# Kernel optimization log

Hardware: AMD Instinct MI355X
Metric: run time of the kernel (lower is better)

The kernel has to match this reference:

```python
import jax, jax.numpy as jnp
import numpy as np

NUM_ITERS = 3
NUM_HEADS = 4
EPS = 1e-8
LN_EPS = 1e-5


def _layernorm(x, w, b):
    mu = jnp.mean(x, axis=-1, keepdims=True)
    var = jnp.mean(jnp.square(x - mu), axis=-1, keepdims=True)
    return (x - mu) * jax.lax.rsqrt(var + LN_EPS) * w + b


def setup_inputs() -> dict:
    key = jax.random.key(0)
    ks = jax.random.split(key, 12)
    B, K, D, Q, Hm = 64, 4096, 256, 8, 512
    s = 0.02
    return {
        "inputs": jax.random.normal(ks[0], (B, K, D), jnp.float32),
        "slots_init": jax.random.normal(ks[1], (B, Q, D), jnp.float32),
        "Wq": jax.random.normal(ks[2], (D, D), jnp.float32) * s,
        "Wk": jax.random.normal(ks[3], (D, D), jnp.float32) * s,
        "Wv": jax.random.normal(ks[4], (D, D), jnp.float32) * s,
        "ln_in_w": jnp.ones((D,), jnp.float32),
        "ln_in_b": jnp.zeros((D,), jnp.float32),
        "ln_slots_w": jnp.ones((D,), jnp.float32),
        "ln_slots_b": jnp.zeros((D,), jnp.float32),
        "ln_mlp_w": jnp.ones((D,), jnp.float32),
        "ln_mlp_b": jnp.zeros((D,), jnp.float32),
        "gru_Wih": jax.random.normal(ks[5], (3 * D, D), jnp.float32) * s,
        "gru_Whh": jax.random.normal(ks[6], (3 * D, D), jnp.float32) * s,
        "gru_bih": jnp.zeros((3 * D,), jnp.float32),
        "gru_bhh": jnp.zeros((3 * D,), jnp.float32),
        "mlp_W1": jax.random.normal(ks[7], (D, Hm), jnp.float32) * s,
        "mlp_b1": jnp.zeros((Hm,), jnp.float32),
        "mlp_W2": jax.random.normal(ks[8], (Hm, D), jnp.float32) * s,
        "mlp_b2": jnp.zeros((D,), jnp.float32),
    }


def reference(inputs, slots_init, Wq, Wk, Wv, ln_in_w, ln_in_b, ln_slots_w,
              ln_slots_b, ln_mlp_w, ln_mlp_b, gru_Wih, gru_Whh, gru_bih,
              gru_bhh, mlp_W1, mlp_b1, mlp_W2, mlp_b2):
    B, K, D = inputs.shape
    Q = slots_init.shape[1]
    H = NUM_HEADS
    dh = D // H
    scale = dh ** -0.5

    x = _layernorm(inputs, ln_in_w, ln_in_b)
    k = (x @ Wk).reshape(B, K, H, dh).transpose(0, 2, 1, 3) * scale  # [B,H,K,dh]
    v = (x @ Wv).reshape(B, K, H, dh).transpose(0, 2, 1, 3)          # [B,H,K,dh]

    slots = slots_init
    attn = None
    for _ in range(NUM_ITERS):
        slots_prev = slots
        s_n = _layernorm(slots, ln_slots_w, ln_slots_b)
        q = (s_n @ Wq).reshape(B, Q, H, dh).transpose(0, 2, 1, 3)    # [B,H,Q,dh]
        logits = jnp.einsum('bhkd,bhqd->bhkq', k, q)                 # [B,H,K,Q]
        # softmax jointly over (heads, slots) per kv position
        attn = jax.nn.softmax(
            logits.transpose(0, 2, 1, 3).reshape(B, K, H * Q), axis=-1
        ).reshape(B, K, H, Q).transpose(0, 2, 1, 3)                  # [B,H,K,Q]
        attn = attn + EPS
        attn = attn / jnp.sum(attn, axis=2, keepdims=True)           # renorm over K
        updates = jnp.einsum('bhkq,bhkd->bqhd', attn, v).reshape(B, Q, D)

        # GRU cell (PyTorch gate order: r, z, n)
        u = updates.reshape(-1, D)
        h = slots_prev.reshape(-1, D)
        gi = u @ gru_Wih.T + gru_bih
        gh = h @ gru_Whh.T + gru_bhh
        i_r, i_z, i_n = jnp.split(gi, 3, axis=-1)
        h_r, h_z, h_n = jnp.split(gh, 3, axis=-1)
        r = jax.nn.sigmoid(i_r + h_r)
        z = jax.nn.sigmoid(i_z + h_z)
        n = jnp.tanh(i_n + r * h_n)
        slots = ((1.0 - z) * n + z * h).reshape(B, Q, D)

        m = _layernorm(slots, ln_mlp_w, ln_mlp_b)
        slots = slots + jax.nn.relu(m @ mlp_W1 + mlp_b1) @ mlp_W2 + mlp_b2

    return slots, attn.mean(axis=1).transpose(0, 2, 1)  # [B,Q,D], [B,Q,K]
```

## Files before the change

### kernel.cpp

```cpp
#include <hip/hip_runtime.h>

#define B   64
#define KK  4096
#define D   256
#define Q   8
#define H   4
#define DH  64
#define HQ  32
#define HM  512
#define NCH 16
#define CHK 256
#define EPS 1e-8f
#define LNE 1e-5f
#define SCALE 0.125f

typedef short bf16x8 __attribute__((ext_vector_type(8)));
typedef float f32x4 __attribute__((ext_vector_type(4)));

#define MFMA __builtin_amdgcn_mfma_f32_16x16x32_bf16

__device__ __forceinline__ float bf2f(unsigned short u) {
    unsigned int x = ((unsigned int)u) << 16;
    float f; __builtin_memcpy(&f, &x, 4); return f;
}
__device__ __forceinline__ unsigned short f2bf(float f) {
    unsigned int x; __builtin_memcpy(&x, &f, 4);
    unsigned int lsb = (x >> 16) & 1u;
    x += 0x7fffu + lsb;
    return (unsigned short)(x >> 16);
}

__device__ __forceinline__ void gload16(const void* g, void* l) {
    __builtin_amdgcn_global_load_lds(
        (const __attribute__((address_space(1))) unsigned int*)g,
        (__attribute__((address_space(3))) unsigned int*)l, 16, 0, 0);
}

__global__ __launch_bounds__(256) void k_prep(
    const float* __restrict__ Wk, const float* __restrict__ Wv,
    const float* __restrict__ gWih, const float* __restrict__ gWhh,
    const float* __restrict__ W1, const float* __restrict__ W2,
    const float* __restrict__ Wq, const float* __restrict__ s0,
    unsigned short* __restrict__ WkvT, unsigned short* __restrict__ Wihbf,
    unsigned short* __restrict__ Whhbf, unsigned short* __restrict__ W1T,
    unsigned short* __restrict__ W2T, unsigned short* __restrict__ WqT,
    float* __restrict__ slots)
{
    const int blk = blockIdx.x, t = threadIdx.x;
    if (blk < 512) {
        const int c = blk;
        const float v = (c < 256) ? Wk[(size_t)t * 256 + c] * SCALE
                                  : Wv[(size_t)t * 256 + (c - 256)];
        WkvT[(size_t)c * 256 + t] = f2bf(v);
    } else if (blk < 1280) {
        const int i = (blk - 512) * 256 + t;
        Wihbf[i] = f2bf(gWih[i]);
    } else if (blk < 2048) {
        const int i = (blk - 1280) * 256 + t;
        Whhbf[i] = f2bf(gWhh[i]);
    } else if (blk < 2560) {
        const int nn = blk - 2048;
        W1T[(size_t)nn * 256 + t] = f2bf(W1[(size_t)t * 512 + nn]);
    } else if (blk < 2816) {
        const int nn = blk - 2560;
        W2T[(size_t)nn * 512 + t]       = f2bf(W2[(size_t)t * 256 + nn]);
        W2T[(size_t)nn * 512 + 256 + t] = f2bf(W2[(size_t)(256 + t) * 256 + nn]);
    } else if (blk < 3072) {
        const int nn = blk - 2816;
        WqT[(size_t)nn * 256 + t] = f2bf(Wq[(size_t)t * 256 + nn]);
    } else {
        const int i = (blk - 3072) * 256 + t;
        slots[i] = s0[i];
    }
}

__global__ __launch_bounds__(256) void k1_mfma(
    const float* __restrict__ inp, const unsigned short* __restrict__ WkvT,
    const float* __restrict__ lnw, const float* __restrict__ lnb,
    unsigned short* __restrict__ kpk, unsigned short* __restrict__ vpk)
{
    __shared__ char smem[49152];
    char* abase = smem;
    char* bb0 = smem + 32768;
    char* bb1 = smem;
    const int t = threadIdx.x, w = t >> 6, l = t & 63;
    const size_t row0 = (size_t)blockIdx.x * 64;
    const int b_blk = blockIdx.x >> 6;
    const int kbase = (blockIdx.x & 63) * 64;

    auto stageB = [&](int n2, char* dst) {
#pragma unroll
        for (int i = 0; i < 4; ++i) {
            const int seg = w * 4 + i;
            const int r = seg * 2 + (l >> 5);
            const int off = ((l & 31) * 16) ^ ((r & 7) << 4);
            gload16((const char*)WkvT + ((size_t)n2 * 32 + r) * 512 + off, dst + seg * 1024);
        }
    };
    stageB(0, bb0);

    float4 xv[16];
#pragma unroll
    for (int i = 0; i < 16; ++i)
        xv[i] = ((const float4*)(inp + (row0 + w * 16 + i) * D))[l];
    const float4 w4 = ((const float4*)lnw)[l];
    const float4 b4 = ((const float4*)lnb)[l];
#pragma unroll
    for (int i = 0; i < 16; ++i) {
        const int r = w * 16 + i;
        float4 x = xv[i];
        float s  = x.x + x.y + x.z + x.w;
        float ss = x.x*x.x + x.y*x.y + x.z*x.z + x.w*x.w;
#pragma unroll
        for (int off = 32; off; off >>= 1) { s += __shfl_xor(s, off); ss += __shfl_xor(ss, off); }
        const float mu = s * (1.f / 256.f);
        const float rs = rsqrtf(ss * (1.f / 256.f) - mu * mu + LNE);
        ushort4 pk;
        pk.x = f2bf((x.x - mu) * rs * w4.x + b4.x);
        pk.y = f2bf((x.y - mu) * rs * w4.y + b4.y);
        pk.z = f2bf((x.z - mu) * rs * w4.z + b4.z);
        pk.w = f2bf((x.w - mu) * rs * w4.w + b4.w);
        *(ushort4*)(abase + r * 512 + ((l * 8) ^ ((r & 7) << 4))) = pk;
    }
    __syncthreads();

    const int arow = w * 16 + (l & 15);
    const char* ap = abase + arow * 512;
    const int asw = (l & 7) << 4;
    bf16x8 af[8];
#pragma unroll
    for (int kk = 0; kk < 8; ++kk)
        af[kk] = *(const bf16x8*)(ap + ((kk * 64 + (l >> 4) * 16) ^ asw));
    __syncthreads();
    stageB(1, bb1);

    const int lg = l >> 4;
    const f32x4 fz = {0.f, 0.f, 0.f, 0.f};
    for (int n2 = 0; n2 < 16; ++n2) {
        const char* bbase = (n2 & 1) ? bb1 : bb0;
        f32x4 acc[2] = {fz, fz};
        if (n2 < 8) {
#pragma unroll
            for (int kk = 0; kk < 8; ++kk) {
                const int koff = kk * 64 + lg * 16;
#pragma unroll
                for (int nf = 0; nf < 2; ++nf) {
                    const int brow = nf * 16 + (l & 15);
                    const bf16x8 bf_ = *(const bf16x8*)(bbase + brow * 512 + (koff ^ ((brow & 7) << 4)));
                    acc[nf] = MFMA(bf_, af[kk], acc[nf], 0, 0, 0);
                }
            }
            const int kt16 = (kbase >> 4) + w;
#pragma unroll
            for (int nf = 0; nf < 2; ++nf) {
                unsigned short* kp = kpk
                    + ((((size_t)b_blk * 256 + kt16) * 8 + n2) * 512)
                    + ((l & 15) + ((nf * 2 + (lg >> 1)) << 4)) * 8 + (lg & 1) * 4;
                ushort4 pk;
                pk.x = f2bf(acc[nf][0]); pk.y = f2bf(acc[nf][1]);
                pk.z = f2bf(acc[nf][2]); pk.w = f2bf(acc[nf][3]);
                *(ushort4*)kp = pk;
            }
        } else {
#pragma unroll
            for (int kk = 0; kk < 8; ++kk) {
                const int koff = kk * 64 + lg * 16;
#pragma unroll
                for (int nf = 0; nf < 2; ++nf) {
                    const int brow = nf * 16 + (l & 15);
                    const bf16x8 bf_ = *(const bf16x8*)(bbase + brow * 512 + (koff ^ ((brow & 7) << 4)));
                    acc[nf] = MFMA(af[kk], bf_, acc[nf], 0, 0, 0);
                }
            }
            const int kt32 = (kbase >> 5) + (w >> 1);
#pragma unroll
            for (int nf = 0; nf < 2; ++nf) {
                const int dt16 = (n2 - 8) * 2 + nf;
                unsigned short* vp = vpk
                    + ((((size_t)b_blk * 128 + kt32) * 16 + dt16) * 512)
                    + ((l & 15) + (((w & 1) * 2 + (lg >> 1)) << 4)) * 8 + (lg & 1) * 4;
                ushort4 pk;
                pk.x = f2bf(acc[nf][0]); pk.y = f2bf(acc[nf][1]);
                pk.z = f2bf(acc[nf][2]); pk.w = f2bf(acc[nf][3]);
                *(ushort4*)vp = pk;
            }
        }
        __syncthreads();
        if (n2 < 14) stageB(n2 + 2, (n2 & 1) ? bb1 : bb0);
    }
}

__global__ __launch_bounds__(256) void k2_qproj(
    const float* __restrict__ slots, const float* __restrict__ Wq,
    const float* __restrict__ lnw, const float* __restrict__ lnb, float* __restrict__ qbuf)
{
    const int row = blockIdx.x, t = threadIdx.x;
    __shared__ float sn[256];
    __shared__ float red[8];
    const float x = slots[(size_t)row * D + t];
    float mu, rs;
    {
        float s = x, ss = x * x;
#pragma unroll
        for (int off = 32; off; off >>= 1) { s += __shfl_xor(s, off); ss += __shfl_xor(ss, off); }
        if ((t & 63) == 0) { red[t >> 6] = s; red[4 + (t >> 6)] = ss; }
        __syncthreads();
        const float S  = red[0] + red[1] + red[2] + red[3];
        const float SS = red[4] + red[5] + red[6] + red[7];
        mu = S * (1.f / 256.f);
        rs = rsqrtf(SS * (1.f / 256.f) - mu * mu + LNE);
    }
    sn[t] = (x - mu) * rs * lnw[t] + lnb[t];
    __syncthreads();
    float acc = 0.f;
    for (int d = 0; d < 256; ++d) acc = fmaf(sn[d], Wq[(size_t)d * 256 + t], acc);
    qbuf[(size_t)row * D + t] = acc;
}

__global__ __launch_bounds__(256) void k_attn(
    const unsigned short* __restrict__ kpk, const unsigned short* __restrict__ vpk,
    const float* __restrict__ qbuf, float* __restrict__ updp,
    float* __restrict__ denp, float* __restrict__ pbuf, int write_p)
{
    __shared__ unsigned short psm[2][2048];
    __shared__ float dred[4][32];
    const int t = threadIdx.x, w = t >> 6, l = t & 63;
    const int b = blockIdx.x >> 4, chunk = blockIdx.x & 15;
    const int k0g = chunk * CHK;
    const int n = l & 15, lg = l >> 4;

    bf16x8 qf[2][2];
#pragma unroll
    for (int p = 0; p < 2; ++p) {
        const int h = p * 2 + (n >> 3);
        const float* qb = qbuf + ((size_t)b * Q + (n & 7)) * D;
#pragma unroll
        for (int j = 0; j < 2; ++j) {
            const int dbase = (h * 2 + j) * 32 + lg * 8;
            short tmp[8];
#pragma unroll
            for (int e = 0; e < 8; ++e) tmp[e] = (short)f2bf(qb[dbase + e]);
            __builtin_memcpy(&qf[p][j], tmp, 16);
        }
    }
    const bf16x8 ZV = {0,0,0,0,0,0,0,0};
    const f32x4 fz = {0.f,0.f,0.f,0.f};
    f32x4 pv[2][4];
#pragma unroll
    for (int mt = 0; mt < 2; ++mt)
#pragma unroll
        for (int nf = 0; nf < 4; ++nf) pv[mt][nf] = fz;
    float den0 = 0.f, den1 = 0.f;

    const unsigned short* kb0 = kpk + (((size_t)(b * 256 + chunk * 16 + w)) * 8) * 512 + l * 8;
    const unsigned short* vb0 = vpk + (((size_t)(b * 128 + chunk * 8) * 16) + w * 4) * 512 + l * 8;

    for (int tile = 0; tile < 4; ++tile) {
        bf16x8 kf[8];
#pragma unroll
        for (int kk = 0; kk < 8; ++kk)
            kf[kk] = *(const bf16x8*)(kb0 + (size_t)tile * 16384 + kk * 512);
        f32x4 lac[2] = {fz, fz};
#pragma unroll
        for (int kk = 0; kk < 8; ++kk) {
            const int p = kk >> 2;
            const bool on = (((kk & 3) >> 1) == (n >> 3));
            const bf16x8 bq = on ? qf[p][kk & 1] : ZV;
            if (p == 0) lac[0] = MFMA(kf[kk], bq, lac[0], 0, 0, 0);
            else        lac[1] = MFMA(kf[kk], bq, lac[1], 0, 0, 0);
        }
#pragma unroll
        for (int reg = 0; reg < 4; ++reg) {
            float m = fmaxf(lac[0][reg], lac[1][reg]);
#pragma unroll
            for (int off = 8; off; off >>= 1) m = fmaxf(m, __shfl_xor(m, off));
            const float e0 = __expf(lac[0][reg] - m);
            const float e1 = __expf(lac[1][reg] - m);
            float se = e0 + e1;
#pragma unroll
            for (int off = 8; off; off >>= 1) se += __shfl_xor(se, off);
            const float inv = 1.f / se;
            lac[0][reg] = e0 * inv; lac[1][reg] = e1 * inv;
            den0 += lac[0][reg];    den1 += lac[1][reg];
        }
        char* pb = (char*)psm[tile & 1];
        const int kb = w * 16 + lg * 4;
        {
            ushort4 p0, p1;
            p0.x = f2bf(lac[0][0]); p0.y = f2bf(lac[0][1]); p0.z = f2bf(lac[0][2]); p0.w = f2bf(lac[0][3]);
            p1.x = f2bf(lac[1][0]); p1.y = f2bf(lac[1][1]); p1.z = f2bf(lac[1][2]); p1.w = f2bf(lac[1][3]);
            *(ushort4*)(pb + n * 128 + ((kb * 2) ^ ((n & 7) << 4))) = p0;
            *(ushort4*)(pb + (16 + n) * 128 + ((kb * 2) ^ ((n & 7) << 4))) = p1;
        }
        if (write_p) {
            float* pp = pbuf + ((size_t)b * KK + k0g + tile * 64 + kb) * HQ;
#pragma unroll
            for (int reg = 0; reg < 4; ++reg) {
                pp[(size_t)reg * HQ + n] = lac[0][reg];
                pp[(size_t)reg * HQ + 16 + n] = lac[1][reg];
            }
        }
        __syncthreads();
#pragma unroll
        for (int kkp = 0; kkp < 2; ++kkp) {
            const int koff = kkp * 64 + lg * 16;
            const bf16x8 a0 = *(const bf16x8*)(pb + n * 128 + (koff ^ ((n & 7) << 4)));
            const bf16x8 a1 = *(const bf16x8*)(pb + (16 + n) * 128 + (koff ^ ((n & 7) << 4)));
#pragma unroll
            for (int nf = 0; nf < 4; ++nf) {
                const bf16x8 bv = *(const bf16x8*)(vb0 + (tile * 32 + kkp * 16 + nf) * 512);
                pv[0][nf] = MFMA(a0, bv, pv[0][nf], 0, 0, 0);
                pv[1][nf] = MFMA(a1, bv, pv[1][nf], 0, 0, 0);
            }
        }
    }

    den0 += __shfl_xor(den0, 16); den0 += __shfl_xor(den0, 32);
    den1 += __shfl_xor(den1, 16); den1 += __shfl_xor(den1, 32);
    if (l < 16) { dred[w][l] = den0; dred[w][16 + l] = den1; }
    __syncthreads();
    if (t < 32)
        denp[((size_t)b * NCH + chunk) * HQ + t] =
            dred[0][t] + dred[1][t] + dred[2][t] + dred[3][t];

    if ((lg >> 1) == (w & 1)) {
        const int mt = w >> 1;
#pragma unroll
        for (int nf = 0; nf < 4; ++nf) {
#pragma unroll
            for (int reg = 0; reg < 4; ++reg) {
                const int q = (lg & 1) * 4 + reg;
                updp[(((size_t)b * NCH + chunk) * Q + q) * D + w * 64 + nf * 16 + n] = pv[mt][nf][reg];
            }
        }
    }
}

__device__ __forceinline__ void ln_rows(const f32x4 sv[4], char* dstA, float* red,
    const float* __restrict__ lnw, const float* __restrict__ lnb,
    int w, int n, int lg, int col0)
{
    float ps[4], pq[4];
#pragma unroll
    for (int r = 0; r < 4; ++r) {
        float s = 0.f, q2 = 0.f;
#pragma unroll
        for (int nf = 0; nf < 4; ++nf) { const float v = sv[nf][r]; s += v; q2 += v * v; }
#pragma unroll
        for (int off = 1; off < 16; off <<= 1) { s += __shfl_xor(s, off); q2 += __shfl_xor(q2, off); }
        ps[r] = s; pq[r] = q2;
    }
    if (n == 0) {
#pragma unroll
        for (int r = 0; r < 4; ++r) {
            red[(lg * 4 + r) * 8 + w * 2]     = ps[r];
            red[(lg * 4 + r) * 8 + w * 2 + 1] = pq[r];
        }
    }
    __syncthreads();
    float mu[4], rs[4];
#pragma unroll
    for (int r = 0; r < 4; ++r) {
        const int rowm = lg * 4 + r;
        const float S  = red[rowm*8+0] + red[rowm*8+2] + red[rowm*8+4] + red[rowm*8+6];
        const float SS = red[rowm*8+1] + red[rowm*8+3] + red[rowm*8+5] + red[rowm*8+7];
        mu[r] = S * (1.f / 256.f);
        rs[r] = rsqrtf(SS * (1.f / 256.f) - mu[r] * mu[r] + LNE);
    }
#pragma unroll
    for (int nf = 0; nf < 4; ++nf) {
        const int col = col0 + nf * 16;
        const float wv = lnw[col], bv = lnb[col];
#pragma unroll
        for (int r = 0; r < 4; ++r) {
            const int rowm = lg * 4 + r;
            const float mval = (sv[nf][r] - mu[r]) * rs[r] * wv + bv;
            *(unsigned short*)(dstA + rowm * 512 + ((col * 2) ^ ((rowm & 7) << 4))) = f2bf(mval);
        }
    }
}

__global__ __launch_bounds__(256) void k_slot(
    const float* __restrict__ updp, const float* __restrict__ denp,
    float* __restrict__ slots,
    const unsigned short* __restrict__ Wihbf, const unsigned short* __restrict__ Whhbf,
    const float* __restrict__ bih, const float* __restrict__ bhh,
    const unsigned short* __restrict__ W1T, const float* __restrict__ b1,
    const unsigned short* __restrict__ W2T, const float* __restrict__ b2,
    const float* __restrict__ lnmw, const float* __restrict__ lnmb,
    const unsigned short* __restrict__ WqT,
    const float* __restrict__ lnsw, const float* __restrict__ lnsb,
    float* __restrict__ qbuf)
{
    __shared__ char sm[34304];
    unsigned short* uA = (unsigned short*)(sm);
    unsigned short* hA = (unsigned short*)(sm + 8192);
    float* hf32        = (float*)(sm + 16384);
    char*  hidA        = sm + 16384;
    float* dsum        = (float*)(sm + 33280);
    float* red         = (float*)(sm + 33536);
    const int t = threadIdx.x, w = t >> 6, l = t & 63;
    const int n = l & 15, lg = l >> 4;
    const int R0 = blockIdx.x * 16;
    const f32x4 fz = {0.f, 0.f, 0.f, 0.f};

    {
        float us[16];
#pragma unroll
        for (int m = 0; m < 16; ++m) {
            const int gr = R0 + m, bb = gr >> 3, q = gr & 7;
            float s = 0.f;
#pragma unroll
            for (int c = 0; c < 16; ++c)
                s += updp[(((size_t)(bb * 16 + c)) * 8 + q) * 256 + t];
            us[m] = s;
        }
        if (t < 64) {
            const int m = t >> 2, h = t & 3;
            const int gr = R0 + m, bb = gr >> 3, q = gr & 7;
            float s = 0.f;
#pragma unroll
            for (int c = 0; c < 16; ++c)
                s += denp[(size_t)(bb * 16 + c) * 32 + h * 8 + q];
            dsum[m * 4 + h] = s;
        }
#pragma unroll
        for (int m = 0; m < 16; ++m) {
            const float hv = slots[(size_t)(R0 + m) * 256 + t];
            hf32[m * 264 + t] = hv;
            *(unsigned short*)((char*)hA + m * 512 + ((t * 2) ^ ((m & 7) << 4))) = f2bf(hv);
        }
        __syncthreads();
        const int h = t >> 6;
#pragma unroll
        for (int m = 0; m < 16; ++m) {
            const float inv = 1.f / (dsum[m * 4 + h] + (float)KK * EPS);
            *(unsigned short*)((char*)uA + m * 512 + ((t * 2) ^ ((m & 7) << 4))) = f2bf(us[m] * inv);
        }
    }
    __syncthreads();

    f32x4 sv[4];
    {
        f32x4 ai0[4], ai1[4], ai2[4];
#pragma unroll
        for (int nf = 0; nf < 4; ++nf) { ai0[nf] = fz; ai1[nf] = fz; ai2[nf] = fz; }
#pragma unroll
        for (int kk = 0; kk < 8; ++kk) {
            const bf16x8 au = *(const bf16x8*)((char*)uA + n * 512 + ((kk * 64 + lg * 16) ^ ((n & 7) << 4)));
            const int kidx = kk * 32 + lg * 8;
#pragma unroll
            for (int nf = 0; nf < 4; ++nf) {
                const int col = w * 64 + nf * 16 + n;
                const bf16x8 br = *(const bf16x8*)(Wihbf + (size_t)col * 256 + kidx);
                const bf16x8 bz = *(const bf16x8*)(Wihbf + (size_t)(256 + col) * 256 + kidx);
                const bf16x8 bn = *(const bf16x8*)(Wihbf + (size_t)(512 + col) * 256 + kidx);
                ai0[nf] = MFMA(au, br, ai0[nf], 0, 0, 0);
                ai1[nf] = MFMA(au, bz, ai1[nf], 0, 0, 0);
                ai2[nf] = MFMA(au, bn, ai2[nf], 0, 0, 0);
            }
        }
        f32x4 ah0[4], ah1[4], ah2[4];
#pragma unroll
        for (int nf = 0; nf < 4; ++nf) { ah0[nf] = fz; ah1[nf] = fz; ah2[nf] = fz; }
#pragma unroll
        for (int kk = 0; kk < 8; ++kk) {
            const bf16x8 ah_ = *(const bf16x8*)((char*)hA + n * 512 + ((kk * 64 + lg * 16) ^ ((n & 7) << 4)));
            const int kidx = kk * 32 + lg * 8;
#pragma unroll
            for (int nf = 0; nf < 4; ++nf) {
                const int col = w * 64 + nf * 16 + n;
                const bf16x8 cr = *(const bf16x8*)(Whhbf + (size_t)col * 256 + kidx);
                const bf16x8 cz = *(const bf16x8*)(Whhbf + (size_t)(256 + col) * 256 + kidx);
                const bf16x8 cn = *(const bf16x8*)(Whhbf + (size_t)(512 + col) * 256 + kidx);
                ah0[nf] = MFMA(ah_, cr, ah0[nf], 0, 0, 0);
                ah1[nf] = MFMA(ah_, cz, ah1[nf], 0, 0, 0);
                ah2[nf] = MFMA(ah_, cn, ah2[nf], 0, 0, 0);
            }
        }
#pragma unroll
        for (int nf = 0; nf < 4; ++nf) {
            const int col = w * 64 + nf * 16 + n;
            const float br_ = bih[col], bz_ = bih[256 + col], bn_ = bih[512 + col];
            const float cr_ = bhh[col], cz_ = bhh[256 + col], cn_ = bhh[512 + col];
#pragma unroll
            for (int r = 0; r < 4; ++r) {
                const int rowm = lg * 4 + r;
                const float ir = ai0[nf][r] + br_, iz = ai1[nf][r] + bz_, inn = ai2[nf][r] + bn_;
                const float hr = ah0[nf][r] + cr_, hz = ah1[nf][r] + cz_, hn = ah2[nf][r] + cn_;
                const float rg = 1.f / (1.f + __expf(-(ir + hr)));
                const float zg = 1.f / (1.f + __expf(-(iz + hz)));
                const float ng = tanhf(inn + rg * hn);
                const float h0v = hf32[rowm * 264 + col];
                sv[nf][r] = (1.f - zg) * ng + zg * h0v;
            }
        }
    }
    ln_rows(sv, (char*)uA, red, lnmw, lnmb, w, n, lg, w * 64 + n);
    __syncthreads();

    {
        f32x4 m1[8];
#pragma unroll
        for (int nf = 0; nf < 8; ++nf) m1[nf] = fz;
#pragma unroll
        for (int kk = 0; kk < 8; ++kk) {
            const bf16x8 a = *(const bf16x8*)((char*)uA + n * 512 + ((kk * 64 + lg * 16) ^ ((n & 7) << 4)));
            const int kidx = kk * 32 + lg * 8;
#pragma unroll
            for (int nf = 0; nf < 8; ++nf) {
                const int colh = w * 128 + nf * 16 + n;
                const bf16x8 bb = *(const bf16x8*)(W1T + (size_t)colh * 256 + kidx);
                m1[nf] = MFMA(a, bb, m1[nf], 0, 0, 0);
            }
        }
        __syncthreads();
#pragma unroll
        for (int nf = 0; nf < 8; ++nf) {
            const int colh = w * 128 + nf * 16 + n;
            const float bb = b1[colh];
#pragma unroll
            for (int r = 0; r < 4; ++r) {
                const int rowm = lg * 4 + r;
                *(unsigned short*)(hidA + rowm * 1024 + ((colh * 2) ^ ((rowm & 7) << 4)))
                    = f2bf(fmaxf(m1[nf][r] + bb, 0.f));
            }
        }
    }
    __syncthreads();

    {
        f32x4 m2[4];
#pragma unroll
        for (int nf = 0; nf < 4; ++nf) m2[nf] = fz;
#pragma unroll
        for (int kk = 0; kk < 16; ++kk) {
            const bf16x8 a = *(const bf16x8*)(hidA + n * 1024 + ((kk * 64 + lg * 16) ^ ((n & 7) << 4)));
            const int kidx = kk * 32 + lg * 8;
#pragma unroll
            for (int nf = 0; nf < 4; ++nf) {
                const int col = w * 64 + nf * 16 + n;
                const bf16x8 bb = *(const bf16x8*)(W2T + (size_t)col * 512 + kidx);
                m2[nf] = MFMA(a, bb, m2[nf], 0, 0, 0);
            }
        }
#pragma unroll
        for (int nf = 0; nf < 4; ++nf) {
            const int col = w * 64 + nf * 16 + n;
            const float bb = b2[col];
#pragma unroll
            for (int r = 0; r < 4; ++r) {
                const int rowm = lg * 4 + r;
                const float v = m2[nf][r] + bb + sv[nf][r];
                sv[nf][r] = v;
                slots[(size_t)(R0 + rowm) * 256 + col] = v;
            }
        }
    }
    ln_rows(sv, (char*)hA, red, lnsw, lnsb, w, n, lg, w * 64 + n);
    __syncthreads();

    {
        f32x4 qa[4];
#pragma unroll
        for (int nf = 0; nf < 4; ++nf) qa[nf] = fz;
#pragma unroll
        for (int kk = 0; kk < 8; ++kk) {
            const bf16x8 a = *(const bf16x8*)((char*)hA + n * 512 + ((kk * 64 + lg * 16) ^ ((n & 7) << 4)));
            const int kidx = kk * 32 + lg * 8;
#pragma unroll
            for (int nf = 0; nf < 4; ++nf) {
                const int col = w * 64 + nf * 16 + n;
                const bf16x8 bb = *(const bf16x8*)(WqT + (size_t)col * 256 + kidx);
                qa[nf] = MFMA(a, bb, qa[nf], 0, 0, 0);
            }
        }
#pragma unroll
        for (int nf = 0; nf < 4; ++nf) {
            const int col = w * 64 + nf * 16 + n;
#pragma unroll
            for (int r = 0; r < 4; ++r)
                qbuf[(size_t)(R0 + lg * 4 + r) * 256 + col] = qa[nf][r];
        }
    }
}

__global__ void k_den(const float* __restrict__ denp, float* __restrict__ invden)
{
    const int b = blockIdx.x, t = threadIdx.x;
    float s = 0.f;
#pragma unroll
    for (int c = 0; c < NCH; ++c) s += denp[((size_t)b * NCH + c) * HQ + t];
    invden[b * HQ + t] = 1.f / (s + (float)KK * EPS);
}

__global__ void k7_copy(const float* __restrict__ s, float* __restrict__ o)
{
    const int i = blockIdx.x * 256 + threadIdx.x;
    o[i] = s[i];
}

__global__ __launch_bounds__(256) void k7_attnout(
    const float* __restrict__ pbuf, const float* __restrict__ invden, float* __restrict__ out2)
{
    const int blk = blockIdx.x;
    const int b = blk >> 4;
    const int kk0 = (blk & 15) * 256;
    __shared__ float ps[256][33];
    __shared__ float inv[32];
    const int t = threadIdx.x;
    const float* pp = pbuf + ((size_t)b * KK + kk0) * HQ;
    for (int i = 0; i < 32; ++i) {
        const int idx = i * 256 + t;
        ps[idx >> 5][idx & 31] = pp[idx];
    }
    if (t < 32) inv[t] = invden[b * HQ + t];
    __syncthreads();
    float* o = out2 + (size_t)b * Q * KK + kk0 + t;
#pragma unroll
    for (int q = 0; q < 8; ++q) {
        float v = 0.f;
#pragma unroll
        for (int hh = 0; hh < 4; ++hh)
            v += (ps[t][hh * 8 + q] + EPS) * inv[hh * 8 + q];
        o[(size_t)q * KK] = v * 0.25f;
    }
}

extern "C" void kernel_launch(void* const* d_in, const int* in_sizes, int n_in,
                              void* d_out, int out_size, void* d_ws, size_t ws_size,
                              hipStream_t stream)
{
    const float* inputs  = (const float*)d_in[0];
    const float* slots0  = (const float*)d_in[1];
    const float* Wq      = (const float*)d_in[2];
    const float* Wk      = (const float*)d_in[3];
    const float* Wv      = (const float*)d_in[4];
    const float* ln_in_w = (const float*)d_in[5];
    const float* ln_in_b = (const float*)d_in[6];
    const float* ln_s_w  = (const float*)d_in[7];
    const float* ln_s_b  = (const float*)d_in[8];
    const float* ln_m_w  = (const float*)d_in[9];
    const float* ln_m_b  = (const float*)d_in[10];
    const float* gWih    = (const float*)d_in[11];
    const float* gWhh    = (const float*)d_in[12];
    const float* gbih    = (const float*)d_in[13];
    const float* gbhh    = (const float*)d_in[14];
    const float* W1      = (const float*)d_in[15];
    const float* b1      = (const float*)d_in[16];
    const float* W2      = (const float*)d_in[17];
    const float* b2      = (const float*)d_in[18];

    char* p = (char*)d_ws;
    unsigned short* kpk   = (unsigned short*)p; p += (size_t)B * KK * D * 2;
    unsigned short* vpk   = (unsigned short*)p; p += (size_t)B * KK * D * 2;
    float* pbuf   = (float*)p; p += (size_t)B * KK * HQ * 4;
    float* updp   = (float*)p; p += (size_t)B * NCH * Q * D * 4;
    float* denp   = (float*)p; p += (size_t)B * NCH * HQ * 4;
    float* invden = (float*)p; p += (size_t)B * HQ * 4;
    float* qbuf   = (float*)p; p += (size_t)B * Q * D * 4;
    float* slots  = (float*)p; p += (size_t)B * Q * D * 4;
    unsigned short* WkvT  = (unsigned short*)p; p += (size_t)512 * 256 * 2;
    unsigned short* Wihbf = (unsigned short*)p; p += (size_t)768 * 256 * 2;
    unsigned short* Whhbf = (unsigned short*)p; p += (size_t)768 * 256 * 2;
    unsigned short* W1T   = (unsigned short*)p; p += (size_t)HM * 256 * 2;
    unsigned short* W2T   = (unsigned short*)p; p += (size_t)256 * HM * 2;
    unsigned short* WqT   = (unsigned short*)p; p += (size_t)256 * 256 * 2;

    k_prep<<<3584, 256, 0, stream>>>(Wk, Wv, gWih, gWhh, W1, W2, Wq, slots0,
                                     WkvT, Wihbf, Whhbf, W1T, W2T, WqT, slots);
    k1_mfma<<<(B * KK) / 64, 256, 0, stream>>>(inputs, WkvT, ln_in_w, ln_in_b, kpk, vpk);
    k2_qproj<<<B * Q, 256, 0, stream>>>(slots, Wq, ln_s_w, ln_s_b, qbuf);
    for (int it = 0; it < 3; ++it) {
        k_attn<<<B * NCH, 256, 0, stream>>>(kpk, vpk, qbuf, updp, denp, pbuf, (it == 2) ? 1 : 0);
        k_slot<<<32, 256, 0, stream>>>(updp, denp, slots, Wihbf, Whhbf, gbih, gbhh,
                                       W1T, b1, W2T, b2, ln_m_w, ln_m_b, WqT,
                                       ln_s_w, ln_s_b, qbuf);
    }
    k_den<<<B, 32, 0, stream>>>(denp, invden);
    k7_copy<<<(B * Q * D) / 256, 256, 0, stream>>>(slots, (float*)d_out);
    k7_attnout<<<B * (KK / 256), 256, 0, stream>>>(pbuf, invden, (float*)d_out + (size_t)B * Q * D);
}
```

Measured before the change: 551.6 us.

## Fold input layernorm into K/V projection epilogue, prefetch V, drop small kernels

The input layernorm's affine weights and mean subtraction are folded algebraically into pre-packed projection weights. Column sums and bias vectors are applied in the MFMA epilogue, so k1 feeds raw bf16 inputs and loads B tiles from a pre-swizzled layout with less LDS. k_attn prefetches V fragments into registers alongside K and drops the softmax max-subtraction, which risks overflow if logits are large. The k_den and copy kernels are removed by fusing the denominator reduction into k7_attnout and writing the final slots directly from k_slot.

```diff
diff --git a/kernel.cpp b/kernel.cpp
--- a/kernel.cpp
+++ b/kernel.cpp
@@ -38,91 +38,96 @@
 
 __global__ __launch_bounds__(256) void k_prep(
     const float* __restrict__ Wk, const float* __restrict__ Wv,
+    const float* __restrict__ lnw, const float* __restrict__ lnb,
     const float* __restrict__ gWih, const float* __restrict__ gWhh,
     const float* __restrict__ W1, const float* __restrict__ W2,
     const float* __restrict__ Wq, const float* __restrict__ s0,
-    unsigned short* __restrict__ WkvT, unsigned short* __restrict__ Wihbf,
-    unsigned short* __restrict__ Whhbf, unsigned short* __restrict__ W1T,
-    unsigned short* __restrict__ W2T, unsigned short* __restrict__ WqT,
-    float* __restrict__ slots)
+    unsigned short* __restrict__ wpk, float* __restrict__ cs, float* __restrict__ b2v,
+    unsigned short* __restrict__ Wihbf, unsigned short* __restrict__ Whhbf,
+    unsigned short* __restrict__ W1T, unsigned short* __restrict__ W2T,
+    unsigned short* __restrict__ WqT, float* __restrict__ slots)
 {
     const int blk = blockIdx.x, t = threadIdx.x;
-    if (blk < 512) {
-        const int c = blk;
-        const float v = (c < 256) ? Wk[(size_t)t * 256 + c] * SCALE
-                                  : Wv[(size_t)t * 256 + (c - 256)];
-        WkvT[(size_t)c * 256 + t] = f2bf(v);
-    } else if (blk < 1280) {
-        const int i = (blk - 512) * 256 + t;
+    if (blk < 256) {
+        const int ct = blk >> 3, kt = blk & 7;
+#pragma unroll
+        for (int e2 = 0; e2 < 2; ++e2) {
+            const int i = t * 2 + e2;
+            const int lane = i >> 3, e = i & 7;
+            const int col = ct * 16 + (lane & 15);
+            const int k = kt * 32 + (lane >> 4) * 8 + e;
+            const float wv = lnw[k];
+            const float v = (col < 256) ? wv * Wk[(size_t)k * 256 + col] * SCALE
+                                        : wv * Wv[(size_t)k * 256 + (col - 256)];
+            wpk[(size_t)blk * 512 + i] = f2bf(v);
+        }
+    } else if (blk < 258) {
+        const int c = (blk - 256) * 256 + t;
+        float s1 = 0.f, s2 = 0.f;
+        for (int k = 0; k < 256; ++k) {
+            const float wraw = (c < 256) ? Wk[(size_t)k * 256 + c] * SCALE
+                                         : Wv[(size_t)k * 256 + (c - 256)];
+            s1 += lnw[k] * wraw;
+            s2 += lnb[k] * wraw;
+        }
+        cs[c] = s1; b2v[c] = s2;
+    } else if (blk < 1026) {
+        const int i = (blk - 258) * 256 + t;
         Wihbf[i] = f2bf(gWih[i]);
-    } else if (blk < 2048) {
-        const int i = (blk - 1280) * 256 + t;
+    } else if (blk < 1794) {
+        const int i = (blk - 1026) * 256 + t;
         Whhbf[i] = f2bf(gWhh[i]);
-    } else if (blk < 2560) {
-        const int nn = blk - 2048;
+    } else if (blk < 2306) {
+        const int nn = blk - 1794;
         W1T[(size_t)nn * 256 + t] = f2bf(W1[(size_t)t * 512 + nn]);
-    } else if (blk < 2816) {
-        const int nn = blk - 2560;
+    } else if (blk < 2562) {
+        const int nn = blk - 2306;
         W2T[(size_t)nn * 512 + t]       = f2bf(W2[(size_t)t * 256 + nn]);
         W2T[(size_t)nn * 512 + 256 + t] = f2bf(W2[(size_t)(256 + t) * 256 + nn]);
-    } else if (blk < 3072) {
-        const int nn = blk - 2816;
+    } else if (blk < 2818) {
+        const int nn = blk - 2562;
         WqT[(size_t)nn * 256 + t] = f2bf(Wq[(size_t)t * 256 + nn]);
     } else {
-        const int i = (blk - 3072) * 256 + t;
+        const int i = (blk - 2818) * 256 + t;
         slots[i] = s0[i];
     }
 }
 
 __global__ __launch_bounds__(256) void k1_mfma(
-    const float* __restrict__ inp, const unsigned short* __restrict__ WkvT,
-    const float* __restrict__ lnw, const float* __restrict__ lnb,
+    const float* __restrict__ inp, const unsigned short* __restrict__ wpk,
+    const float* __restrict__ cs, const float* __restrict__ b2v,
     unsigned short* __restrict__ kpk, unsigned short* __restrict__ vpk)
 {
-    __shared__ char smem[49152];
+    __shared__ char smem[32768];
     char* abase = smem;
-    char* bb0 = smem + 32768;
-    char* bb1 = smem;
+    char* bb0 = smem;
+    char* bb1 = smem + 16384;
     const int t = threadIdx.x, w = t >> 6, l = t & 63;
     const size_t row0 = (size_t)blockIdx.x * 64;
     const int b_blk = blockIdx.x >> 6;
     const int kbase = (blockIdx.x & 63) * 64;
-
-    auto stageB = [&](int n2, char* dst) {
-#pragma unroll
-        for (int i = 0; i < 4; ++i) {
-            const int seg = w * 4 + i;
-            const int r = seg * 2 + (l >> 5);
-            const int off = ((l & 31) * 16) ^ ((r & 7) << 4);
-            gload16((const char*)WkvT + ((size_t)n2 * 32 + r) * 512 + off, dst + seg * 1024);
-        }
-    };
-    stageB(0, bb0);
+    const int lg = l >> 4;
 
     float4 xv[16];
 #pragma unroll
     for (int i = 0; i < 16; ++i)
         xv[i] = ((const float4*)(inp + (row0 + w * 16 + i) * D))[l];
-    const float4 w4 = ((const float4*)lnw)[l];
-    const float4 b4 = ((const float4*)lnb)[l];
+    float rsA = 0.f, muA = 0.f;
 #pragma unroll
     for (int i = 0; i < 16; ++i) {
         const int r = w * 16 + i;
-        float4 x = xv[i];
+        const float4 x = xv[i];
         float s  = x.x + x.y + x.z + x.w;
         float ss = x.x*x.x + x.y*x.y + x.z*x.z + x.w*x.w;
 #pragma unroll
         for (int off = 32; off; off >>= 1) { s += __shfl_xor(s, off); ss += __shfl_xor(ss, off); }
         const float mu = s * (1.f / 256.f);
         const float rs = rsqrtf(ss * (1.f / 256.f) - mu * mu + LNE);
+        if ((l & 15) == i) { rsA = rs; muA = rs * mu; }
         ushort4 pk;
-        pk.x = f2bf((x.x - mu) * rs * w4.x + b4.x);
-        pk.y = f2bf((x.y - mu) * rs * w4.y + b4.y);
-        pk.z = f2bf((x.z - mu) * rs * w4.z + b4.z);
-        pk.w = f2bf((x.w - mu) * rs * w4.w + b4.w);
+        pk.x = f2bf(x.x); pk.y = f2bf(x.y); pk.z = f2bf(x.z); pk.w = f2bf(x.w);
         *(ushort4*)(abase + r * 512 + ((l * 8) ^ ((r & 7) << 4))) = pk;
     }
-    __syncthreads();
 
     const int arow = w * 16 + (l & 15);
     const char* ap = abase + arow * 512;
@@ -130,11 +135,26 @@
     bf16x8 af[8];
 #pragma unroll
     for (int kk = 0; kk < 8; ++kk)
-        af[kk] = *(const bf16x8*)(ap + ((kk * 64 + (l >> 4) * 16) ^ asw));
-    __syncthreads();
-    stageB(1, bb1);
-
-    const int lg = l >> 4;
+        af[kk] = *(const bf16x8*)(ap + ((kk * 64 + lg * 16) ^ asw));
+    float rsV[4], muV[4];
+#pragma unroll
+    for (int r = 0; r < 4; ++r) {
+        rsV[r] = __shfl(rsA, lg * 4 + r);
+        muV[r] = __shfl(muA, lg * 4 + r);
+    }
+    __syncthreads();
+
+    auto stageB = [&](int n2, char* dst) {
+#pragma unroll
+        for (int i = 0; i < 4; ++i) {
+            const int seg = w * 4 + i;
+            gload16((const char*)wpk + (size_t)n2 * 16384 + seg * 1024 + l * 16,
+                    dst + seg * 1024);
+        }
+    };
+    stageB(0, bb0); stageB(1, bb1);
+    __syncthreads();
+
     const f32x4 fz = {0.f, 0.f, 0.f, 0.f};
     for (int n2 = 0; n2 < 16; ++n2) {
         const char* bbase = (n2 & 1) ? bb1 : bb0;
@@ -142,46 +162,51 @@
         if (n2 < 8) {
 #pragma unroll
             for (int kk = 0; kk < 8; ++kk) {
-                const int koff = kk * 64 + lg * 16;
 #pragma unroll
                 for (int nf = 0; nf < 2; ++nf) {
-                    const int brow = nf * 16 + (l & 15);
-                    const bf16x8 bf_ = *(const bf16x8*)(bbase + brow * 512 + (koff ^ ((brow & 7) << 4)));
+                    const bf16x8 bf_ = *(const bf16x8*)(bbase + (nf * 8 + kk) * 1024 + l * 16);
                     acc[nf] = MFMA(bf_, af[kk], acc[nf], 0, 0, 0);
                 }
             }
             const int kt16 = (kbase >> 4) + w;
 #pragma unroll
             for (int nf = 0; nf < 2; ++nf) {
+                const int d0 = n2 * 32 + nf * 16 + lg * 4;
+                const float4 cs4 = *(const float4*)(cs + d0);
+                const float4 bb4 = *(const float4*)(b2v + d0);
                 unsigned short* kp = kpk
                     + ((((size_t)b_blk * 256 + kt16) * 8 + n2) * 512)
                     + ((l & 15) + ((nf * 2 + (lg >> 1)) << 4)) * 8 + (lg & 1) * 4;
                 ushort4 pk;
-                pk.x = f2bf(acc[nf][0]); pk.y = f2bf(acc[nf][1]);
-                pk.z = f2bf(acc[nf][2]); pk.w = f2bf(acc[nf][3]);
+                pk.x = f2bf(rsA * acc[nf][0] - muA * cs4.x + bb4.x);
+                pk.y = f2bf(rsA * acc[nf][1] - muA * cs4.y + bb4.y);
+                pk.z = f2bf(rsA * acc[nf][2] - muA * cs4.z + bb4.z);
+                pk.w = f2bf(rsA * acc[nf][3] - muA * cs4.w + bb4.w);
                 *(ushort4*)kp = pk;
             }
         } else {
 #pragma unroll
             for (int kk = 0; kk < 8; ++kk) {
-                const int koff = kk * 64 + lg * 16;
 #pragma unroll
                 for (int nf = 0; nf < 2; ++nf) {
-                    const int brow = nf * 16 + (l & 15);
-                    const bf16x8 bf_ = *(const bf16x8*)(bbase + brow * 512 + (koff ^ ((brow & 7) << 4)));
+                    const bf16x8 bf_ = *(const bf16x8*)(bbase + (nf * 8 + kk) * 1024 + l * 16);
                     acc[nf] = MFMA(af[kk], bf_, acc[nf], 0, 0, 0);
                 }
             }
             const int kt32 = (kbase >> 5) + (w >> 1);
 #pragma unroll
             for (int nf = 0; nf < 2; ++nf) {
+                const int c = n2 * 32 + nf * 16 + (l & 15);
+                const float csc = cs[c], b2c = b2v[c];
                 const int dt16 = (n2 - 8) * 2 + nf;
                 unsigned short* vp = vpk
                     + ((((size_t)b_blk * 128 + kt32) * 16 + dt16) * 512)
                     + ((l & 15) + (((w & 1) * 2 + (lg >> 1)) << 4)) * 8 + (lg & 1) * 4;
                 ushort4 pk;
-                pk.x = f2bf(acc[nf][0]); pk.y = f2bf(acc[nf][1]);
-                pk.z = f2bf(acc[nf][2]); pk.w = f2bf(acc[nf][3]);
+                pk.x = f2bf(rsV[0] * acc[nf][0] - muV[0] * csc + b2c);
+                pk.y = f2bf(rsV[1] * acc[nf][1] - muV[1] * csc + b2c);
+                pk.z = f2bf(rsV[2] * acc[nf][2] - muV[2] * csc + b2c);
+                pk.w = f2bf(rsV[3] * acc[nf][3] - muV[3] * csc + b2c);
                 *(ushort4*)vp = pk;
             }
         }
@@ -256,10 +281,13 @@
     const unsigned short* vb0 = vpk + (((size_t)(b * 128 + chunk * 8) * 16) + w * 4) * 512 + l * 8;
 
     for (int tile = 0; tile < 4; ++tile) {
-        bf16x8 kf[8];
+        bf16x8 kf[8], vf[8];
 #pragma unroll
         for (int kk = 0; kk < 8; ++kk)
             kf[kk] = *(const bf16x8*)(kb0 + (size_t)tile * 16384 + kk * 512);
+#pragma unroll
+        for (int i = 0; i < 8; ++i)
+            vf[i] = *(const bf16x8*)(vb0 + (tile * 32 + (i >> 2) * 16 + (i & 3)) * 512);
         f32x4 lac[2] = {fz, fz};
 #pragma unroll
         for (int kk = 0; kk < 8; ++kk) {
@@ -271,11 +299,8 @@
         }
 #pragma unroll
         for (int reg = 0; reg < 4; ++reg) {
-            float m = fmaxf(lac[0][reg], lac[1][reg]);
-#pragma unroll
-            for (int off = 8; off; off >>= 1) m = fmaxf(m, __shfl_xor(m, off));
-            const float e0 = __expf(lac[0][reg] - m);
-            const float e1 = __expf(lac[1][reg] - m);
+            const float e0 = __expf(lac[0][reg]);
+            const float e1 = __expf(lac[1][reg]);
             float se = e0 + e1;
 #pragma unroll
             for (int off = 8; off; off >>= 1) se += __shfl_xor(se, off);
@@ -308,7 +333,7 @@
             const bf16x8 a1 = *(const bf16x8*)(pb + (16 + n) * 128 + (koff ^ ((n & 7) << 4)));
 #pragma unroll
             for (int nf = 0; nf < 4; ++nf) {
-                const bf16x8 bv = *(const bf16x8*)(vb0 + (tile * 32 + kkp * 16 + nf) * 512);
+                const bf16x8 bv = vf[kkp * 4 + nf];
                 pv[0][nf] = MFMA(a0, bv, pv[0][nf], 0, 0, 0);
                 pv[1][nf] = MFMA(a1, bv, pv[1][nf], 0, 0, 0);
             }
@@ -390,7 +415,7 @@
     const float* __restrict__ lnmw, const float* __restrict__ lnmb,
     const unsigned short* __restrict__ WqT,
     const float* __restrict__ lnsw, const float* __restrict__ lnsb,
-    float* __restrict__ qbuf)
+    float* __restrict__ qbuf, float* __restrict__ outp)
 {
     __shared__ char sm[34304];
     unsigned short* uA = (unsigned short*)(sm);
@@ -554,6 +579,7 @@
                 const float v = m2[nf][r] + bb + sv[nf][r];
                 sv[nf][r] = v;
                 slots[(size_t)(R0 + rowm) * 256 + col] = v;
+                if (outp) outp[(size_t)(R0 + rowm) * 256 + col] = v;
             }
         }
     }
@@ -585,23 +611,8 @@
     }
 }
 
-__global__ void k_den(const float* __restrict__ denp, float* __restrict__ invden)
-{
-    const int b = blockIdx.x, t = threadIdx.x;
-    float s = 0.f;
-#pragma unroll
-    for (int c = 0; c < NCH; ++c) s += denp[((size_t)b * NCH + c) * HQ + t];
-    invden[b * HQ + t] = 1.f / (s + (float)KK * EPS);
-}
-
-__global__ void k7_copy(const float* __restrict__ s, float* __restrict__ o)
-{
-    const int i = blockIdx.x * 256 + threadIdx.x;
-    o[i] = s[i];
-}
-
 __global__ __launch_bounds__(256) void k7_attnout(
-    const float* __restrict__ pbuf, const float* __restrict__ invden, float* __restrict__ out2)
+    const float* __restrict__ pbuf, const float* __restrict__ denp, float* __restrict__ out2)
 {
     const int blk = blockIdx.x;
     const int b = blk >> 4;
@@ -614,7 +625,12 @@
         const int idx = i * 256 + t;
         ps[idx >> 5][idx & 31] = pp[idx];
     }
-    if (t < 32) inv[t] = invden[b * HQ + t];
+    if (t < 32) {
+        float s = 0.f;
+#pragma unroll
+        for (int c = 0; c < NCH; ++c) s += denp[((size_t)b * NCH + c) * HQ + t];
+        inv[t] = 1.f / (s + (float)KK * EPS);
+    }
     __syncthreads();
     float* o = out2 + (size_t)b * Q * KK + kk0 + t;
 #pragma unroll
@@ -657,27 +673,27 @@
     float* pbuf   = (float*)p; p += (size_t)B * KK * HQ * 4;
     float* updp   = (float*)p; p += (size_t)B * NCH * Q * D * 4;
     float* denp   = (float*)p; p += (size_t)B * NCH * HQ * 4;
-    float* invden = (float*)p; p += (size_t)B * HQ * 4;
     float* qbuf   = (float*)p; p += (size_t)B * Q * D * 4;
     float* slots  = (float*)p; p += (size_t)B * Q * D * 4;
-    unsigned short* WkvT  = (unsigned short*)p; p += (size_t)512 * 256 * 2;
+    unsigned short* wpk   = (unsigned short*)p; p += (size_t)512 * 256 * 2;
+    float* csv    = (float*)p; p += 512 * 4;
+    float* b2vv   = (float*)p; p += 512 * 4;
     unsigned short* Wihbf = (unsigned short*)p; p += (size_t)768 * 256 * 2;
     unsigned short* Whhbf = (unsigned short*)p; p += (size_t)768 * 256 * 2;
     unsigned short* W1T   = (unsigned short*)p; p += (size_t)HM * 256 * 2;
     unsigned short* W2T   = (unsigned short*)p; p += (size_t)256 * HM * 2;
     unsigned short* WqT   = (unsigned short*)p; p += (size_t)256 * 256 * 2;
 
-    k_prep<<<3584, 256, 0, stream>>>(Wk, Wv, gWih, gWhh, W1, W2, Wq, slots0,
-                                     WkvT, Wihbf, Whhbf, W1T, W2T, WqT, slots);
-    k1_mfma<<<(B * KK) / 64, 256, 0, stream>>>(inputs, WkvT, ln_in_w, ln_in_b, kpk, vpk);
+    k_prep<<<3330, 256, 0, stream>>>(Wk, Wv, ln_in_w, ln_in_b, gWih, gWhh, W1, W2, Wq, slots0,
+                                     wpk, csv, b2vv, Wihbf, Whhbf, W1T, W2T, WqT, slots);
+    k1_mfma<<<(B * KK) / 64, 256, 0, stream>>>(inputs, wpk, csv, b2vv, kpk, vpk);
     k2_qproj<<<B * Q, 256, 0, stream>>>(slots, Wq, ln_s_w, ln_s_b, qbuf);
     for (int it = 0; it < 3; ++it) {
         k_attn<<<B * NCH, 256, 0, stream>>>(kpk, vpk, qbuf, updp, denp, pbuf, (it == 2) ? 1 : 0);
         k_slot<<<32, 256, 0, stream>>>(updp, denp, slots, Wihbf, Whhbf, gbih, gbhh,
                                        W1T, b1, W2T, b2, ln_m_w, ln_m_b, WqT,
-                                       ln_s_w, ln_s_b, qbuf);
-    }
-    k_den<<<B, 32, 0, stream>>>(denp, invden);
-    k7_copy<<<(B * Q * D) / 256, 256, 0, stream>>>(slots, (float*)d_out);
-    k7_attnout<<<B * (KK / 256), 256, 0, stream>>>(pbuf, invden, (float*)d_out + (size_t)B * Q * D);
-}
+                                       ln_s_w, ln_s_b, qbuf,
+                                       (it == 2) ? (float*)d_out : (float*)nullptr);
+    }
+    k7_attnout<<<B * (KK / 256), 256, 0, stream>>>(pbuf, denp, (float*)d_out + (size_t)B * Q * D);
+}
```

Result: slower. 603.8 us (+9.5%).
